# Kernel optimization log

Hardware: AMD Instinct MI355X
Metric: run time of the kernel (lower is better)

The kernel has to match this reference:

```python
import jax, jax.numpy as jnp
import numpy as np

V, E, H, L = 50257, 512, 512, 2
PAD_ID = 50256


def setup_inputs() -> dict:
    key = jax.random.key(0)
    ks = jax.random.split(key, 24)
    B, TD, TE = 16, 64, 256
    s = 0.02
    emb = jax.random.normal(ks[0], (V, E), jnp.float32) * s
    emb = emb.at[PAD_ID].set(0.0)  # padding_idx row is zero
    inp = {
        "dec_input_ids": jax.random.randint(ks[1], (B, TD), 0, V, jnp.int32),
        "initial_hidden": jax.random.normal(ks[2], (L, B, H), jnp.float32),
        "initial_cell": jax.random.normal(ks[3], (L, B, H), jnp.float32),
        "encoder_outputs": jax.random.normal(ks[4], (B, TE, H), jnp.float32),
        "src_mask": jax.random.randint(ks[5], (B, TE), 0, 2, jnp.int32),
        "emb": emb,
        "W1_w": jax.random.normal(ks[6], (H, H), jnp.float32) * s,
        "W1_b": jnp.zeros((H,), jnp.float32),
        "W2_w": jax.random.normal(ks[7], (H, H), jnp.float32) * s,
        "W2_b": jnp.zeros((H,), jnp.float32),
        "v_w": jax.random.normal(ks[8], (H,), jnp.float32) * s,
        "v_b": jnp.zeros((), jnp.float32),
        "W_ih0": jax.random.normal(ks[9], (4 * H, E + H), jnp.float32) * s,
        "W_hh0": jax.random.normal(ks[10], (4 * H, H), jnp.float32) * s,
        "b_ih0": jnp.zeros((4 * H,), jnp.float32),
        "b_hh0": jnp.zeros((4 * H,), jnp.float32),
        "W_ih1": jax.random.normal(ks[11], (4 * H, H), jnp.float32) * s,
        "W_hh1": jax.random.normal(ks[12], (4 * H, H), jnp.float32) * s,
        "b_ih1": jnp.zeros((4 * H,), jnp.float32),
        "b_hh1": jnp.zeros((4 * H,), jnp.float32),
        "fc_w": jax.random.normal(ks[13], (V, H), jnp.float32) * s,
        "fc_b": jnp.zeros((V,), jnp.float32),
    }
    return inp


def _lstm_cell(x, h, c, Wi, Wh, bi, bh):
    g = x @ Wi.T + bi + h @ Wh.T + bh  # (B, 4H)
    i, f, gg, o = jnp.split(g, 4, axis=-1)  # PyTorch gate order i,f,g,o
    i, f, o = jax.nn.sigmoid(i), jax.nn.sigmoid(f), jax.nn.sigmoid(o)
    gg = jnp.tanh(gg)
    cn = f * c + i * gg
    hn = o * jnp.tanh(cn)
    return hn, cn


def reference(dec_input_ids, initial_hidden, initial_cell, encoder_outputs, src_mask,
              emb, W1_w, W1_b, W2_w, W2_b, v_w, v_b,
              W_ih0, W_hh0, b_ih0, b_hh0, W_ih1, W_hh1, b_ih1, b_hh1,
              fc_w, fc_b):
    embedded = emb[dec_input_ids]                      # (B, T_dec, E)
    enc_proj = encoder_outputs @ W1_w.T + W1_b         # W1(encoder_outputs), (B, T_enc, H)
    pad = src_mask == 0                                # (B, T_enc)
    layers = ((W_ih0, W_hh0, b_ih0, b_hh0), (W_ih1, W_hh1, b_ih1, b_hh1))

    def step(carry, emb_t):
        h, c = carry                                   # each (L, B, H)
        q = h[-1] @ W2_w.T + W2_b                      # (B, H)
        score = jnp.tanh(enc_proj + q[:, None, :]) @ v_w + v_b  # (B, T_enc)
        score = jnp.where(pad, -1e9, score)
        attn = jax.nn.softmax(score, axis=-1)
        context = jnp.einsum('bt,bth->bh', attn, encoder_outputs)
        x = jnp.concatenate([emb_t, context], axis=-1)  # (B, E+H)
        hs, cs = [], []
        for l, (Wi, Wh, bi, bh) in enumerate(layers):
            hn, cn = _lstm_cell(x, h[l], c[l], Wi, Wh, bi, bh)
            hs.append(hn); cs.append(cn)
            x = hn
        logits_t = x @ fc_w.T + fc_b                    # (B, V)
        return (jnp.stack(hs), jnp.stack(cs)), logits_t

    _, logits = jax.lax.scan(step, (initial_hidden, initial_cell),
                             jnp.swapaxes(embedded, 0, 1))  # (T_dec, B, V)
    return jnp.swapaxes(logits, 0, 1)                       # (B, T_dec, V)
```

## Files before the change

### kernel.cpp

```cpp
#include <hip/hip_runtime.h>

#define DI __device__ __forceinline__

typedef __attribute__((ext_vector_type(2))) float f32x2;
typedef __attribute__((ext_vector_type(4))) float f32x4;
typedef __attribute__((ext_vector_type(8))) short bf16x8;
typedef __attribute__((ext_vector_type(8))) unsigned short u16x8;

constexpr int Vv = 50257, NPAD = 50304, Ee = 512, Hh = 512, Bb = 16, TDn = 64, TEn = 256;
constexpr int NBLK = 64;

constexpr size_t OFF_ENCP = 0;
constexpr size_t OFF_ENCT = OFF_ENCP + (size_t)Bb*TEn*Hh*4;
constexpr size_t OFF_G0E  = OFF_ENCT + (size_t)Bb*Hh*TEn*4;
constexpr size_t OFF_FCWB = OFF_G0E  + (size_t)TDn*Bb*4*Hh*4;
constexpr size_t OFF_H1B  = OFF_FCWB + (size_t)NPAD*Hh*2;
constexpr size_t OFF_Q    = OFF_H1B  + (size_t)TDn*Bb*Hh*2;
constexpr size_t OFF_SC   = OFF_Q    + (size_t)Bb*Hh*4;
constexpr size_t OFF_CTX  = OFF_SC   + (size_t)Bb*TEn*4;
constexpr size_t OFF_H0   = OFF_CTX  + (size_t)Bb*Hh*4;
constexpr size_t OFF_H1   = OFF_H0   + (size_t)2*Bb*Hh*4;
constexpr size_t OFF_SYNC = OFF_H1   + (size_t)2*Bb*Hh*4;

DI float dot4(f32x4 a, f32x4 b) { return a[0]*b[0] + a[1]*b[1] + a[2]*b[2] + a[3]*b[3]; }
DI float wsum(float v) { for (int m = 32; m; m >>= 1) v += __shfl_xor(v, m, 64); return v; }
DI float wmax(float v) { for (int m = 32; m; m >>= 1) v = fmaxf(v, __shfl_xor(v, m, 64)); return v; }
DI float tanhfast(float x) { float e = __expf(2.f * x); return 1.f - 2.f / (e + 1.f); }
DI float sigm(float x) { return 1.f / (1.f + __expf(-x)); }

template<int NV>
DI float xreduce(float (&buf)[NV], const int l) {
    int cnt = NV;
    #pragma unroll
    for (int m = 1; m < NV; m <<= 1) {
        const bool hi = (l & m) != 0;
        #pragma unroll
        for (int i = 0; i < NV; ++i) {
            if (i < cnt / 2) {
                float x0 = buf[2*i], x1 = buf[2*i + 1];
                float send = hi ? x0 : x1;
                float keep = hi ? x1 : x0;
                float recv = __shfl_xor(send, m, 64);
                buf[i] = keep + recv;
            }
        }
        cnt >>= 1;
    }
    float v = buf[0];
    #pragma unroll
    for (int m = NV; m < 64; m <<= 1)
        v += __shfl_xor(v, m, 64);
    return v;
}

DI int swz(int a) { return a ^ (((a >> 5) & 7) << 2); }

DI float gload1(const float* p) {
    return __hip_atomic_load(p, __ATOMIC_RELAXED, __HIP_MEMORY_SCOPE_AGENT);
}
DI void gstore1(float* p, float v) {
    __hip_atomic_store(p, v, __ATOMIC_RELAXED, __HIP_MEMORY_SCOPE_AGENT);
}
DI f32x2 gload2(const float* p) {
    unsigned long long u = __hip_atomic_load((const unsigned long long*)p,
                                             __ATOMIC_RELAXED, __HIP_MEMORY_SCOPE_AGENT);
    return __builtin_bit_cast(f32x2, u);
}
DI void gstore2(float* p, f32x2 v) {
    __hip_atomic_store((unsigned long long*)p, __builtin_bit_cast(unsigned long long, v),
                       __ATOMIC_RELAXED, __HIP_MEMORY_SCOPE_AGENT);
}
DI f32x4 gload4(const float* p) {
    f32x2 a = gload2(p), b = gload2(p + 2);
    f32x4 r; r[0] = a[0]; r[1] = a[1]; r[2] = b[0]; r[3] = b[1];
    return r;
}
DI void gstoreu16(unsigned short* p, unsigned short v) {
    __hip_atomic_store(p, v, __ATOMIC_RELAXED, __HIP_MEMORY_SCOPE_AGENT);
}

DI unsigned short f2bf(float f) {
    unsigned u = __builtin_bit_cast(unsigned, f);
    unsigned r = (u + 0x7FFFu + ((u >> 16) & 1u)) >> 16;
    return (unsigned short)r;
}
DI u16x8 cvt8(f32x4 a, f32x4 b) {
    u16x8 r;
    r[0]=f2bf(a[0]); r[1]=f2bf(a[1]); r[2]=f2bf(a[2]); r[3]=f2bf(a[3]);
    r[4]=f2bf(b[0]); r[5]=f2bf(b[1]); r[6]=f2bf(b[2]); r[7]=f2bf(b[3]);
    return r;
}

DI void gbar(char* sy, int bid, unsigned kg) {
    __syncthreads();
    unsigned* fl = (unsigned*)(sy + ((kg & 1) ? 0 : 8192));
    const int tid = threadIdx.x;
    if (tid == 0) {
        asm volatile("s_waitcnt vmcnt(0)" ::: "memory");
        __hip_atomic_store(fl + (size_t)bid * 32, kg, __ATOMIC_RELAXED, __HIP_MEMORY_SCOPE_AGENT);
    }
    if (tid < 64) {
        bool done = false;
        for (;;) {
            if (!done)
                done = (__hip_atomic_load(fl + (size_t)tid * 32, __ATOMIC_RELAXED,
                                          __HIP_MEMORY_SCOPE_AGENT) == kg);
            if (__all(done)) break;
            __builtin_amdgcn_s_sleep(32);
        }
    }
    __syncthreads();
}

DI void rbar(char* sy, int gb, int u4, unsigned kr) {
    __syncthreads();
    if (threadIdx.x == 0) {
        unsigned* w = (unsigned*)(sy + ((kr & 1) ? 16384 : 18432)) + (size_t)gb * 32;
        asm volatile("s_waitcnt vmcnt(0)" ::: "memory");
        __hip_atomic_store((char*)w + u4, (char)(unsigned char)kr, __ATOMIC_RELAXED,
                           __HIP_MEMORY_SCOPE_AGENT);
        const unsigned pat = 0x01010101u * (unsigned char)kr;
        while (__hip_atomic_load(w, __ATOMIC_RELAXED, __HIP_MEMORY_SCOPE_AGENT) != pat)
            __builtin_amdgcn_s_sleep(8);
    }
    __syncthreads();
}

__global__ void prep_fcw_kernel(const float* __restrict__ src, unsigned short* __restrict__ dst) {
    size_t i = ((size_t)blockIdx.x * 256 + threadIdx.x) << 3;
    int n = (int)(i >> 9);
    u16x8 v = {0,0,0,0,0,0,0,0};
    if (n < Vv) {
        const float* p = src + i;
        v = cvt8(*(const f32x4*)p, *(const f32x4*)(p + 4));
    }
    *(u16x8*)(dst + i) = v;
}

__global__ void transpose_kernel(const float* __restrict__ enc, float* __restrict__ encT) {
    __shared__ float tile[32][33];
    const int b = blockIdx.z, e0 = blockIdx.x << 5, h0 = blockIdx.y << 5;
    const int tx = threadIdx.x, ty = threadIdx.y;
    #pragma unroll
    for (int i = 0; i < 4; ++i)
        tile[ty + i*8][tx] = enc[((size_t)(b*TEn + e0 + ty + i*8))*Hh + h0 + tx];
    __syncthreads();
    #pragma unroll
    for (int i = 0; i < 4; ++i)
        encT[((size_t)(b*Hh + h0 + ty + i*8))*TEn + e0 + tx] = tile[tx][ty + i*8];
}

template<int SRCBF, int GATHER, int OUTM>
__global__ __launch_bounds__(256, 2) void gemm_bt(
    const void* __restrict__ Av, const void* __restrict__ Bv,
    const float* __restrict__ bias, const float* __restrict__ bias2,
    float* __restrict__ Cout, int M, int N, int K, int ldb,
    const int* __restrict__ ids, int NV)
{
    __shared__ unsigned short As[128*32], Bs[128*32];
    const int tid = threadIdx.x;
    const int bn = blockIdx.x, bm = blockIdx.y;
    const int w = tid >> 6, l = tid & 63;
    const int wm = w >> 1, wn = w & 1;
    const int lr = l & 15, ls = l >> 4;
    f32x4 acc[4][4] = {};

    const int r0 = tid >> 2, c0 = (tid & 3) << 3;

    for (int kb = 0; kb < K; kb += 32) {
        #pragma unroll
        for (int half = 0; half < 2; ++half) {
            const int rr = r0 + half*64;
            {
                const int gm = bm*128 + rr;
                size_t arow = GATHER ? (size_t)ids[((gm & 15) << 6) + (gm >> 4)] : (size_t)gm;
                u16x8 v;
                if (SRCBF) {
                    v = *(const u16x8*)((const unsigned short*)Av + arow*(size_t)K + kb + c0);
                } else {
                    const float* ap = (const float*)Av + arow*(size_t)K + kb + c0;
                    v = cvt8(*(const f32x4*)ap, *(const f32x4*)(ap + 4));
                }
                *(u16x8*)&As[rr*32 + c0] = v;
            }
            {
                const size_t brow = (size_t)(bn*128 + rr);
                u16x8 v;
                if (SRCBF) {
                    v = *(const u16x8*)((const unsigned short*)Bv + brow*(size_t)ldb + kb + c0);
                } else {
                    const float* bp = (const float*)Bv + brow*(size_t)ldb + kb + c0;
                    v = cvt8(*(const f32x4*)bp, *(const f32x4*)(bp + 4));
                }
                *(u16x8*)&Bs[rr*32 + c0] = v;
            }
        }
        __syncthreads();
        bf16x8 af[4], bfv[4];
        #pragma unroll
        for (int mt = 0; mt < 4; ++mt) af[mt]  = *(const bf16x8*)&As[(wm*64 + mt*16 + lr)*32 + ls*8];
        #pragma unroll
        for (int nt = 0; nt < 4; ++nt) bfv[nt] = *(const bf16x8*)&Bs[(wn*64 + nt*16 + lr)*32 + ls*8];
        #pragma unroll
        for (int mt = 0; mt < 4; ++mt)
            #pragma unroll
            for (int nt = 0; nt < 4; ++nt)
                acc[mt][nt] = __builtin_amdgcn_mfma_f32_16x16x32_bf16(af[mt], bfv[nt], acc[mt][nt], 0, 0, 0);
        __syncthreads();
    }

    #pragma unroll
    for (int mt = 0; mt < 4; ++mt) {
        #pragma unroll
        for (int nt = 0; nt < 4; ++nt) {
            const int n = bn*128 + wn*64 + nt*16 + lr;
            const int mbase = bm*128 + wm*64 + mt*16 + ls*4;
            f32x4 a = acc[mt][nt];
            #pragma unroll
            for (int r = 0; r < 4; ++r) {
                const int m = mbase + r;
                if (OUTM == 0) {
                    float v = a[r] + bias[n] + (bias2 ? bias2[n] : 0.f);
                    Cout[(size_t)m*N + n] = v;
                } else {
                    if (n < NV) {
                        float v = a[r] + bias[n];
                        Cout[(size_t)(((m & 15) << 6) + (m >> 4))*NV + n] = v;
                    }
                }
            }
        }
    }
}

__global__ __launch_bounds__(512, 2) void recur_kernel(
    const float* __restrict__ ih, const float* __restrict__ ic,
    const float* __restrict__ W2w, const float* __restrict__ W2b,
    const float* __restrict__ vw, const float* __restrict__ vb,
    const int* __restrict__ smask,
    const float* __restrict__ Wi0, const float* __restrict__ Wh0,
    const float* __restrict__ Wi1, const float* __restrict__ Wh1,
    const float* __restrict__ bi1, const float* __restrict__ bh1,
    char* __restrict__ ws)
{
    float* encP = (float*)(ws + OFF_ENCP);
    float* encT = (float*)(ws + OFF_ENCT);
    float* g0e  = (float*)(ws + OFF_G0E);
    unsigned short* h1bf = (unsigned short*)(ws + OFF_H1B);
    float* qb  = (float*)(ws + OFF_Q);
    float* sc  = (float*)(ws + OFF_SC);
    float* ctx = (float*)(ws + OFF_CTX);
    float* h0b = (float*)(ws + OFF_H0);
    float* h1v = (float*)(ws + OFF_H1);
    char* sy   = (char*)(ws + OFF_SYNC);

    __shared__ float lds[2 * Bb * Hh];

    const int tid = threadIdx.x, bid = blockIdx.x;
    const int wid = tid >> 6, l = tid & 63;
    const int j  = (bid << 3) + wid;
    const int k0 = l << 3;

    f32x4 wi0a[4], wi0b[4], wh0a[4], wh0b[4];
    f32x4 wi1a[4], wi1b[4], wh1a[4], wh1b[4];
    float bb1[4];
    #pragma unroll
    for (int g = 0; g < 4; ++g) {
        const float* p0 = Wi0 + (size_t)(g*Hh + j)*(Ee + Hh) + Ee + k0;
        wi0a[g] = *(const f32x4*)p0; wi0b[g] = *(const f32x4*)(p0 + 4);
        const float* p1 = Wh0 + (size_t)(g*Hh + j)*Hh + k0;
        wh0a[g] = *(const f32x4*)p1; wh0b[g] = *(const f32x4*)(p1 + 4);
        const float* p2 = Wi1 + (size_t)(g*Hh + j)*Hh + k0;
        wi1a[g] = *(const f32x4*)p2; wi1b[g] = *(const f32x4*)(p2 + 4);
        const float* p3 = Wh1 + (size_t)(g*Hh + j)*Hh + k0;
        wh1a[g] = *(const f32x4*)p3; wh1b[g] = *(const f32x4*)(p3 + 4);
        bb1[g] = bi1[g*Hh + j] + bh1[g*Hh + j];
    }
    const float* wr = W2w + (size_t)j*Hh + k0;
    const f32x4 w2a = *(const f32x4*)wr, w2d = *(const f32x4*)(wr + 4);
    const float w2bias = W2b[j];
    const f32x4 va = *(const f32x4*)&vw[k0], vd = *(const f32x4*)&vw[k0 + 4];
    const float vbias = vb[0];

    const bool cellLane = ((l & 3) == 0) && (l < 32);
    const int  bA = l >> 2;
    float c0r[2], c1r[2];
    c0r[0] = cellLane ? ic[bA*Hh + j]              : 0.f;
    c0r[1] = cellLane ? ic[(8 + bA)*Hh + j]        : 0.f;
    c1r[0] = cellLane ? ic[Bb*Hh + bA*Hh + j]      : 0.f;
    c1r[1] = cellLane ? ic[Bb*Hh + (8 + bA)*Hh + j]: 0.f;

    const int gb  = bid & 15, u4 = bid >> 4;
    const int se0 = u4*64 + wid*8;
    const int ch0 = u4*128 + wid*16;
    const int msk = (l < 8) ? smask[gb*TEn + se0 + l] : 1;

    for (int i = (bid*512 + tid)*4; i < Bb*Hh; i += NBLK*512*4) {
        gstore2(&h0b[i],     *(const f32x2*)&ih[i]);
        gstore2(&h0b[i + 2], *(const f32x2*)&ih[i + 2]);
        gstore2(&h1v[i],     *(const f32x2*)&ih[Bb*Hh + i]);
        gstore2(&h1v[i + 2], *(const f32x2*)&ih[Bb*Hh + i + 2]);
    }
    unsigned kg = 1, kr = 0;
    gbar(sy, bid, kg);

    for (int t = 0; t < TDn; ++t) {
        const int p = t & 1;
        const float* h1r = h1v + p*(Bb*Hh);
        float*       h1w = h1v + (p^1)*(Bb*Hh);
        const float* h0r = h0b + p*(Bb*Hh);
        float*       h0w = h0b + (p^1)*(Bb*Hh);

        float ge[2][4] = {};
        if (cellLane) {
            const float* gpA = g0e + ((size_t)(t*Bb + bA))*(4*Hh) + j;
            const float* gpB = g0e + ((size_t)(t*Bb + 8 + bA))*(4*Hh) + j;
            #pragma unroll
            for (int g = 0; g < 4; ++g) { ge[0][g] = gpA[(size_t)g*Hh]; ge[1][g] = gpB[(size_t)g*Hh]; }
        }

        {
            for (int i = tid*4; i < Bb*Hh; i += 2048)
                *(f32x4*)&lds[swz(i)] = gload4(&h1r[i]);
            __syncthreads();
            float a[16];
            #pragma unroll
            for (int b = 0; b < Bb; ++b) {
                f32x4 ha = *(const f32x4*)&lds[swz(b*Hh + k0)];
                f32x4 hd = *(const f32x4*)&lds[swz(b*Hh + k0 + 4)];
                a[b] = dot4(ha, w2a) + dot4(hd, w2d);
            }
            float qv = xreduce<16>(a, l) + w2bias;
            if (l < 16) gstore1(&qb[l*Hh + j], qv);
        }
        gbar(sy, bid, ++kg);

        {
            if (tid < 128) *(f32x4*)&lds[tid*4] = gload4(&qb[gb*Hh + tid*4]);
            __syncthreads();
            f32x4 qa = *(const f32x4*)&lds[k0];
            f32x4 qd = *(const f32x4*)&lds[k0 + 4];
            float a[8];
            #pragma unroll
            for (int i = 0; i < 8; ++i) {
                const float* ep = encP + ((size_t)(gb*TEn + se0 + i))*Hh + k0;
                f32x4 ea = *(const f32x4*)ep, ed = *(const f32x4*)(ep + 4);
                float s = 0.f;
                #pragma unroll
                for (int c = 0; c < 4; ++c)
                    s += tanhfast(ea[c] + qa[c]) * va[c] + tanhfast(ed[c] + qd[c]) * vd[c];
                a[i] = s;
            }
            float sv = xreduce<8>(a, l) + vbias;
            if (l < 8)
                gstore1(&sc[gb*TEn + se0 + l], (msk == 0) ? -1e9f : sv);
        }
        rbar(sy, gb, u4, ++kr);

        {
            f32x4 s4 = gload4(&sc[gb*TEn + (l << 2)]);
            float mx = wmax(fmaxf(fmaxf(s4[0], s4[1]), fmaxf(s4[2], s4[3])));
            f32x4 e4; float sm = 0.f;
            #pragma unroll
            for (int c = 0; c < 4; ++c) { e4[c] = __expf(s4[c] - mx); sm += e4[c]; }
            sm = wsum(sm);
            const float inv = 1.0f / sm;
            float a[16];
            #pragma unroll
            for (int i = 0; i < 16; ++i) {
                f32x4 en = *(const f32x4*)&encT[((size_t)(gb*Hh + ch0 + i))*TEn + (l << 2)];
                a[i] = dot4(e4, en);
            }
            float cv = xreduce<16>(a, l) * inv;
            if (l < 16) gstore1(&ctx[gb*Hh + ch0 + l], cv);
        }
        gbar(sy, bid, ++kg);

        {
            for (int i = tid*4; i < Bb*Hh; i += 2048) {
                *(f32x4*)&lds[swz(i)]          = gload4(&ctx[i]);
                *(f32x4*)&lds[swz(Bb*Hh + i)]  = gload4(&h0r[i]);
            }
            __syncthreads();
            #pragma unroll
            for (int pass = 0; pass < 2; ++pass) {
                const int base = pass * 8;
                float acc[32];
                #pragma unroll
                for (int bb = 0; bb < 8; ++bb) {
                    const int b = base + bb;
                    f32x4 xa = *(const f32x4*)&lds[swz(b*Hh + k0)];
                    f32x4 xd = *(const f32x4*)&lds[swz(b*Hh + k0 + 4)];
                    f32x4 ha = *(const f32x4*)&lds[swz(Bb*Hh + b*Hh + k0)];
                    f32x4 hd = *(const f32x4*)&lds[swz(Bb*Hh + b*Hh + k0 + 4)];
                    #pragma unroll
                    for (int g = 0; g < 4; ++g)
                        acc[bb*4 + g] = dot4(wi0a[g],xa) + dot4(wi0b[g],xd)
                                      + dot4(wh0a[g],ha) + dot4(wh0b[g],hd);
                }
                float v  = xreduce<32>(acc, l);
                float x1 = __shfl_xor(v, 1, 64);
                float x2 = __shfl_xor(v, 2, 64);
                float x3 = __shfl_xor(v, 3, 64);
                if (cellLane) {
                    const int b = base + bA;
                    float ii = sigm(v  + ge[pass][0]);
                    float ff = sigm(x1 + ge[pass][1]);
                    float gg = tanhfast(x2 + ge[pass][2]);
                    float oo = sigm(x3 + ge[pass][3]);
                    float cn = ff*c0r[pass] + ii*gg;
                    c0r[pass] = cn;
                    gstore1(&h0w[b*Hh + j], oo * tanhfast(cn));
                }
            }
        }
        gbar(sy, bid, ++kg);

        {
            for (int i = tid*4; i < Bb*Hh; i += 2048) {
                *(f32x4*)&lds[swz(i)]          = gload4(&h0w[i]);
                *(f32x4*)&lds[swz(Bb*Hh + i)]  = gload4(&h1r[i]);
            }
            __syncthreads();
            #pragma unroll
            for (int pass = 0; pass < 2; ++pass) {
                const int base = pass * 8;
                float acc[32];
                #pragma unroll
                for (int bb = 0; bb < 8; ++bb) {
                    const int b = base + bb;
                    f32x4 xa = *(const f32x4*)&lds[swz(b*Hh + k0)];
                    f32x4 xd = *(const f32x4*)&lds[swz(b*Hh + k0 + 4)];
                    f32x4 ha = *(const f32x4*)&lds[swz(Bb*Hh + b*Hh + k0)];
                    f32x4 hd = *(const f32x4*)&lds[swz(Bb*Hh + b*Hh + k0 + 4)];
                    #pragma unroll
                    for (int g = 0; g < 4; ++g)
                        acc[bb*4 + g] = dot4(wi1a[g],xa) + dot4(wi1b[g],xd)
                                      + dot4(wh1a[g],ha) + dot4(wh1b[g],hd);
                }
                float v  = xreduce<32>(acc, l);
                float x1 = __shfl_xor(v, 1, 64);
                float x2 = __shfl_xor(v, 2, 64);
                float x3 = __shfl_xor(v, 3, 64);
                if (cellLane) {
                    const int b = base + bA;
                    float ii = sigm(v  + bb1[0]);
                    float ff = sigm(x1 + bb1[1]);
                    float gg = tanhfast(x2 + bb1[2]);
                    float oo = sigm(x3 + bb1[3]);
                    float cn = ff*c1r[pass] + ii*gg;
                    c1r[pass] = cn;
                    float hn = oo * tanhfast(cn);
                    gstore1(&h1w[b*Hh + j], hn);
                    gstoreu16(&h1bf[((size_t)(t*Bb + b))*Hh + j], f2bf(hn));
                }
            }
        }
        gbar(sy, bid, ++kg);
    }
}

extern "C" void kernel_launch(void* const* d_in, const int* in_sizes, int n_in,
                              void* d_out, int out_size, void* d_ws, size_t ws_size,
                              hipStream_t stream)
{
    const int*   ids  = (const int*)d_in[0];
    const float* ih   = (const float*)d_in[1];
    const float* ic   = (const float*)d_in[2];
    const float* enc  = (const float*)d_in[3];
    const int*   smask= (const int*)d_in[4];
    const float* emb  = (const float*)d_in[5];
    const float* W1w  = (const float*)d_in[6];
    const float* W1b  = (const float*)d_in[7];
    const float* W2w  = (const float*)d_in[8];
    const float* W2b  = (const float*)d_in[9];
    const float* vw   = (const float*)d_in[10];
    const float* vb   = (const float*)d_in[11];
    const float* Wi0  = (const float*)d_in[12];
    const float* Wh0  = (const float*)d_in[13];
    const float* bi0  = (const float*)d_in[14];
    const float* bh0  = (const float*)d_in[15];
    const float* Wi1  = (const float*)d_in[16];
    const float* Wh1  = (const float*)d_in[17];
    const float* bi1  = (const float*)d_in[18];
    const float* bh1  = (const float*)d_in[19];
    const float* fcw  = (const float*)d_in[20];
    const float* fcb  = (const float*)d_in[21];
    float* out = (float*)d_out;
    char*  ws  = (char*)d_ws;

    hipMemsetAsync(ws + OFF_SYNC, 0, 20480, stream);

    prep_fcw_kernel<<<dim3((unsigned)((size_t)NPAD*Hh/8/256)), dim3(256), 0, stream>>>(
        fcw, (unsigned short*)(ws + OFF_FCWB));

    transpose_kernel<<<dim3(TEn/32, Hh/32, Bb), dim3(32, 8), 0, stream>>>(
        enc, (float*)(ws + OFF_ENCT));

    gemm_bt<0,0,0><<<dim3(Hh/128, (Bb*TEn)/128), dim3(256), 0, stream>>>(
        enc, W1w, W1b, nullptr, (float*)(ws + OFF_ENCP),
        Bb*TEn, Hh, Hh, Hh, nullptr, 0);

    gemm_bt<0,1,0><<<dim3((4*Hh)/128, (TDn*Bb)/128), dim3(256), 0, stream>>>(
        emb, Wi0, bi0, bh0, (float*)(ws + OFF_G0E),
        TDn*Bb, 4*Hh, Ee, Ee + Hh, ids, 0);

    {
        void* args[] = { (void*)&ih, (void*)&ic, (void*)&W2w, (void*)&W2b,
                         (void*)&vw, (void*)&vb, (void*)&smask,
                         (void*)&Wi0, (void*)&Wh0, (void*)&Wi1, (void*)&Wh1,
                         (void*)&bi1, (void*)&bh1, (void*)&ws };
        hipLaunchCooperativeKernel((void*)recur_kernel, dim3(NBLK), dim3(512), args, 0, stream);
    }

    gemm_bt<1,0,1><<<dim3(NPAD/128, (TDn*Bb)/128), dim3(256), 0, stream>>>(
        ws + OFF_H1B, ws + OFF_FCWB, fcb, nullptr, out,
        TDn*Bb, NPAD, Hh, Hh, nullptr, Vv);
}
```

Baseline: 3.579 ms.

## Replace grid barrier with group barrier for query projection and use centralized gbar

Recomputes the attention query so that each 4-block group computes q for its own batch row, keeping 16 W2 rows per wave in registers. The step then needs only the small per-batch rbar instead of a full 64-block grid barrier. The grid barrier itself becomes a byte-packed arrive array polled by block 0, which then broadcasts a generation flag, and sleep intervals are shortened. Together these aim to cut synchronisation latency in the serial recurrence, at the cost of many more registers per thread, with launch bounds lowered to one block per SIMD group.

```diff
diff --git a/kernel.cpp b/kernel.cpp
--- a/kernel.cpp
+++ b/kernel.cpp
@@ -93,21 +93,35 @@
 
 DI void gbar(char* sy, int bid, unsigned kg) {
     __syncthreads();
-    unsigned* fl = (unsigned*)(sy + ((kg & 1) ? 0 : 8192));
+    const size_t pofs = (kg & 1) ? 0 : 1024;
+    unsigned long long* arr = (unsigned long long*)(sy + pofs);
+    unsigned* gen = (unsigned*)(sy + 2048 + pofs);
     const int tid = threadIdx.x;
     if (tid == 0) {
         asm volatile("s_waitcnt vmcnt(0)" ::: "memory");
-        __hip_atomic_store(fl + (size_t)bid * 32, kg, __ATOMIC_RELAXED, __HIP_MEMORY_SCOPE_AGENT);
-    }
-    if (tid < 64) {
-        bool done = false;
-        for (;;) {
-            if (!done)
-                done = (__hip_atomic_load(fl + (size_t)tid * 32, __ATOMIC_RELAXED,
-                                          __HIP_MEMORY_SCOPE_AGENT) == kg);
-            if (__all(done)) break;
-            __builtin_amdgcn_s_sleep(32);
-        }
+        char* p = (char*)(arr + (size_t)(bid >> 3) * 16) + (bid & 7);
+        __hip_atomic_store(p, (char)(unsigned char)kg, __ATOMIC_RELAXED, __HIP_MEMORY_SCOPE_AGENT);
+    }
+    if (bid == 0) {
+        if (tid < 64) {
+            const unsigned long long pat = 0x0101010101010101ULL * (unsigned char)kg;
+            for (;;) {
+                bool ok = true;
+                if (tid < 8)
+                    ok = (__hip_atomic_load(arr + (size_t)tid * 16, __ATOMIC_RELAXED,
+                                            __HIP_MEMORY_SCOPE_AGENT) == pat);
+                if (__all(ok)) break;
+                __builtin_amdgcn_s_sleep(2);
+            }
+            asm volatile("" ::: "memory");
+            if (tid < 8)
+                __hip_atomic_store(gen + (size_t)tid * 32, kg, __ATOMIC_RELAXED,
+                                   __HIP_MEMORY_SCOPE_AGENT);
+        }
+    } else if (tid == 0) {
+        unsigned* gp = gen + (size_t)(bid & 7) * 32;
+        while (__hip_atomic_load(gp, __ATOMIC_RELAXED, __HIP_MEMORY_SCOPE_AGENT) != kg)
+            __builtin_amdgcn_s_sleep(2);
     }
     __syncthreads();
 }
@@ -115,13 +129,14 @@
 DI void rbar(char* sy, int gb, int u4, unsigned kr) {
     __syncthreads();
     if (threadIdx.x == 0) {
-        unsigned* w = (unsigned*)(sy + ((kr & 1) ? 16384 : 18432)) + (size_t)gb * 32;
+        const size_t pofs = (kr & 1) ? 4096 : 6144;
+        unsigned* w = (unsigned*)(sy + pofs) + (size_t)gb * 32;
         asm volatile("s_waitcnt vmcnt(0)" ::: "memory");
         __hip_atomic_store((char*)w + u4, (char)(unsigned char)kr, __ATOMIC_RELAXED,
                            __HIP_MEMORY_SCOPE_AGENT);
         const unsigned pat = 0x01010101u * (unsigned char)kr;
         while (__hip_atomic_load(w, __ATOMIC_RELAXED, __HIP_MEMORY_SCOPE_AGENT) != pat)
-            __builtin_amdgcn_s_sleep(8);
+            __builtin_amdgcn_s_sleep(2);
     }
     __syncthreads();
 }
@@ -233,7 +248,7 @@
     }
 }
 
-__global__ __launch_bounds__(512, 2) void recur_kernel(
+__global__ __launch_bounds__(512, 1) void recur_kernel(
     const float* __restrict__ ih, const float* __restrict__ ic,
     const float* __restrict__ W2w, const float* __restrict__ W2b,
     const float* __restrict__ vw, const float* __restrict__ vb,
@@ -276,11 +291,22 @@
         wh1a[g] = *(const f32x4*)p3; wh1b[g] = *(const f32x4*)(p3 + 4);
         bb1[g] = bi1[g*Hh + j] + bh1[g*Hh + j];
     }
-    const float* wr = W2w + (size_t)j*Hh + k0;
-    const f32x4 w2a = *(const f32x4*)wr, w2d = *(const f32x4*)(wr + 4);
-    const float w2bias = W2b[j];
     const f32x4 va = *(const f32x4*)&vw[k0], vd = *(const f32x4*)&vw[k0 + 4];
     const float vbias = vb[0];
+
+    const int gb = bid & 15, u4 = bid >> 4;
+    const int se0 = u4*64 + wid*8;
+    const int ch0 = u4*128 + wid*16;
+    const int msk = (l < 8) ? smask[gb*TEn + se0 + l] : 1;
+
+    const int qrow0 = u4*128 + wid*16;
+    f32x4 w2fa[16], w2fb[16];
+    #pragma unroll
+    for (int r = 0; r < 16; ++r) {
+        const float* wp = W2w + (size_t)(qrow0 + r)*Hh + k0;
+        w2fa[r] = *(const f32x4*)wp; w2fb[r] = *(const f32x4*)(wp + 4);
+    }
+    const float w2bias = W2b[qrow0 + (l & 15)];
 
     const bool cellLane = ((l & 3) == 0) && (l < 32);
     const int  bA = l >> 2;
@@ -290,11 +316,6 @@
     c1r[0] = cellLane ? ic[Bb*Hh + bA*Hh + j]      : 0.f;
     c1r[1] = cellLane ? ic[Bb*Hh + (8 + bA)*Hh + j]: 0.f;
 
-    const int gb  = bid & 15, u4 = bid >> 4;
-    const int se0 = u4*64 + wid*8;
-    const int ch0 = u4*128 + wid*16;
-    const int msk = (l < 8) ? smask[gb*TEn + se0 + l] : 1;
-
     for (int i = (bid*512 + tid)*4; i < Bb*Hh; i += NBLK*512*4) {
         gstore2(&h0b[i],     *(const f32x2*)&ih[i]);
         gstore2(&h0b[i + 2], *(const f32x2*)&ih[i + 2]);
@@ -320,20 +341,16 @@
         }
 
         {
-            for (int i = tid*4; i < Bb*Hh; i += 2048)
-                *(f32x4*)&lds[swz(i)] = gload4(&h1r[i]);
-            __syncthreads();
+            f32x4 h1a = gload4(&h1r[gb*Hh + k0]);
+            f32x4 h1d = gload4(&h1r[gb*Hh + k0 + 4]);
             float a[16];
             #pragma unroll
-            for (int b = 0; b < Bb; ++b) {
-                f32x4 ha = *(const f32x4*)&lds[swz(b*Hh + k0)];
-                f32x4 hd = *(const f32x4*)&lds[swz(b*Hh + k0 + 4)];
-                a[b] = dot4(ha, w2a) + dot4(hd, w2d);
-            }
+            for (int r = 0; r < 16; ++r)
+                a[r] = dot4(w2fa[r], h1a) + dot4(w2fb[r], h1d);
             float qv = xreduce<16>(a, l) + w2bias;
-            if (l < 16) gstore1(&qb[l*Hh + j], qv);
-        }
-        gbar(sy, bid, ++kg);
+            if (l < 16) gstore1(&qb[gb*Hh + qrow0 + l], qv);
+        }
+        rbar(sy, gb, u4, ++kr);
 
         {
             if (tid < 128) *(f32x4*)&lds[tid*4] = gload4(&qb[gb*Hh + tid*4]);
@@ -489,7 +506,7 @@
     float* out = (float*)d_out;
     char*  ws  = (char*)d_ws;
 
-    hipMemsetAsync(ws + OFF_SYNC, 0, 20480, stream);
+    hipMemsetAsync(ws + OFF_SYNC, 0, 8192, stream);
 
     prep_fcw_kernel<<<dim3((unsigned)((size_t)NPAD*Hh/8/256)), dim3(256), 0, stream>>>(
         fcw, (unsigned short*)(ws + OFF_FCWB));
```

Result: slower. 4.700 ms (+31.3%).
